# Kernel optimization log

Hardware: AMD Instinct MI355X
Metric: run time of the kernel (lower is better)

## Reference

```python
import jax, jax.numpy as jnp
import numpy as np

B, D = 4096, 512
N_PROTO = 1000          # prototype tasks
CLS_PER_TASK = 10       # indices*10 block size in original code
N_CLASSES = N_PROTO * CLS_PER_TASK
NUM_TEST = 10


def setup_inputs() -> dict:
    key = jax.random.key(0)
    k1, k2, k3 = jax.random.split(key, 3)
    img = jax.random.normal(k1, (B, D), dtype=jnp.float32)
    # image encoder output is L2-normalized and detached in the original
    image_features = img / jnp.linalg.norm(img, axis=-1, keepdims=True)
    ima_proto = jax.random.normal(k2, (N_PROTO, D), dtype=jnp.float32)
    ima_proto = ima_proto / jnp.linalg.norm(ima_proto, axis=-1, keepdims=True)
    text_features_raw = jax.random.normal(k3, (N_CLASSES, D), dtype=jnp.float32)
    logit_scale = jnp.asarray(np.log(1.0 / 0.07), dtype=jnp.float32)  # CLIP init
    return {
        "image_features": image_features,
        "ima_proto": ima_proto,
        "text_features_raw": text_features_raw,
        "logit_scale": logit_scale,
        "num_test": NUM_TEST,
    }


def reference(image_features, ima_proto, text_features_raw, logit_scale, num_test):
    n_proto = ima_proto.shape[0]
    n_classes = text_features_raw.shape[0]
    b = image_features.shape[0]
    k = min(int(num_test), n_proto)

    # probability = image_features @ ima_proto.t(); topk indices
    probability = image_features @ ima_proto.T                      # [B, n_proto]
    _, indices = jax.lax.top_k(probability, k)                      # [B, k]

    # text_features normalized, logit = image_features @ text_features.t()
    text_features = text_features_raw / jnp.linalg.norm(
        text_features_raw, axis=-1, keepdims=True)
    logit = image_features @ text_features.T                        # [B, n_classes]

    # vectorized form of the double loop:
    #   logits[j][idx*10 : idx*10+10] = logit[j][idx*10 : idx*10+10]
    sel = jnp.zeros((b, n_proto), dtype=logit.dtype)
    sel = sel.at[jnp.arange(b)[:, None], indices].set(1.0)          # [B, n_proto]
    block_of_class = jnp.arange(n_classes) // CLS_PER_TASK          # [n_classes]
    mask = sel[:, block_of_class]                                   # [B, n_classes]

    logits = jnp.exp(logit_scale) * (logit * mask)
    return logits
```

## Files before the change

kernel.cpp:

```cpp
#include <hip/hip_runtime.h>
#include <cfloat>
#include <math.h>

#define B_ROWS   4096
#define DIM      512
#define NPROTO   1000
#define NCLASSES 10000
#define KSEL     10
#define KCAND    12
#define CAP      256
#define PROB_LD  1024

#define PROB_BYTES 8388608u
#define OUT_BYTES  163840000u

#define GBM 64
#define GBN 128
#define GBK 32
#define ALD 40

typedef short s16x8 __attribute__((ext_vector_type(8)));
typedef float f32x4 __attribute__((ext_vector_type(4)));

static __device__ __forceinline__ unsigned short f2bf(float f) {
  unsigned int x = __float_as_uint(f);
  return (unsigned short)((x + 0x7fffu + ((x >> 16) & 1u)) >> 16);
}
static __device__ __forceinline__ s16x8 cvt8(float4 a, float4 b) {
  s16x8 r;
  r[0]=f2bf(a.x); r[1]=f2bf(a.y); r[2]=f2bf(a.z); r[3]=f2bf(a.w);
  r[4]=f2bf(b.x); r[5]=f2bf(b.y); r[6]=f2bf(b.z); r[7]=f2bf(b.w);
  return r;
}
static __device__ __forceinline__ unsigned short f2h(float f) {
  _Float16 h = (_Float16)f;
  return __builtin_bit_cast(unsigned short, h);
}
static __device__ __forceinline__ unsigned mono16(unsigned h) {
  return (h & 0x8000u) ? (~h & 0xffffu) : (h | 0x8000u);
}

__global__ __launch_bounds__(256) void k_gemm(
    const float* __restrict__ img, const float* __restrict__ proto,
    unsigned short* __restrict__ prob, int* __restrict__ counts)
{
  __shared__ short Al[GBM * ALD];
  __shared__ short Bl[GBN * ALD];

  const int tid  = threadIdx.x;
  const int lane = tid & 63, wave = tid >> 6;
  const int wr = wave >> 1, wc = wave & 1;
  const int row0 = blockIdx.x * GBM;
  const int col0 = blockIdx.y * GBN;

  const int sr = tid >> 2;
  const int sc = (tid & 3) * 8;

  int pa = col0 + sr;      if (pa > NPROTO - 1) pa = NPROTO - 1;
  int pb = col0 + 64 + sr; if (pb > NPROTO - 1) pb = NPROTO - 1;
  const float* gA  = img   + (size_t)(row0 + sr) * DIM + sc;
  const float* gB0 = proto + (size_t)pa * DIM + sc;
  const float* gB1 = proto + (size_t)pb * DIM + sc;

  float4 ra0  = *(const float4*)(gA);      float4 ra1  = *(const float4*)(gA + 4);
  float4 rb00 = *(const float4*)(gB0);     float4 rb01 = *(const float4*)(gB0 + 4);
  float4 rb10 = *(const float4*)(gB1);     float4 rb11 = *(const float4*)(gB1 + 4);

  f32x4 acc[2][4];
#pragma unroll
  for (int m = 0; m < 2; ++m)
#pragma unroll
    for (int n = 0; n < 4; ++n) acc[m][n] = (f32x4)0.f;

  const int kg = lane >> 4;
  const int fr = lane & 15;

  for (int kt = 0; kt < DIM / GBK; ++kt) {
    *(s16x8*)&Al[sr * ALD + sc]        = cvt8(ra0, ra1);
    *(s16x8*)&Bl[sr * ALD + sc]        = cvt8(rb00, rb01);
    *(s16x8*)&Bl[(64 + sr) * ALD + sc] = cvt8(rb10, rb11);
    __syncthreads();

    if (kt + 1 < DIM / GBK) {
      const int k0 = (kt + 1) * GBK;
      ra0  = *(const float4*)(gA + k0);   ra1  = *(const float4*)(gA + k0 + 4);
      rb00 = *(const float4*)(gB0 + k0);  rb01 = *(const float4*)(gB0 + k0 + 4);
      rb10 = *(const float4*)(gB1 + k0);  rb11 = *(const float4*)(gB1 + k0 + 4);
    }

    s16x8 af[2], bf[4];
#pragma unroll
    for (int m = 0; m < 2; ++m)
      af[m] = *(const s16x8*)&Al[(wr * 32 + m * 16 + fr) * ALD + kg * 8];
#pragma unroll
    for (int n = 0; n < 4; ++n)
      bf[n] = *(const s16x8*)&Bl[(wc * 64 + n * 16 + fr) * ALD + kg * 8];
#pragma unroll
    for (int m = 0; m < 2; ++m)
#pragma unroll
      for (int n = 0; n < 4; ++n)
        acc[m][n] = __builtin_amdgcn_mfma_f32_16x16x32_bf16(
            af[m], bf[n], acc[m][n], 0, 0, 0);
    __syncthreads();
  }

#pragma unroll
  for (int m = 0; m < 2; ++m)
#pragma unroll
    for (int n = 0; n < 4; ++n) {
      const int r = row0 + wr * 32 + m * 16 + (lane >> 4) * 4;
      const int c = col0 + wc * 64 + n * 16 + fr;
#pragma unroll
      for (int reg = 0; reg < 4; ++reg)
        prob[(size_t)(r + reg) * PROB_LD + c] = f2h(acc[m][n][reg]);
    }

  if (blockIdx.x == 0 && blockIdx.y == 0)
    for (int i = tid; i < NPROTO; i += 256) counts[i] = 0;
}

__global__ __launch_bounds__(256) void k_select(
    const unsigned short* __restrict__ prob, const float* __restrict__ img,
    const float* __restrict__ proto, int* __restrict__ counts,
    int* __restrict__ buckets)
{
  const int tid  = threadIdx.x;
  const int wave = tid >> 6, lane = tid & 63;
  const int row  = blockIdx.x * 4 + wave;

  unsigned cand[16];
  {
    const uint4* pu = reinterpret_cast<const uint4*>(
        prob + (size_t)row * PROB_LD) + lane * 2;
    const uint4 w0 = pu[0], w1 = pu[1];
    const unsigned w[8] = {w0.x, w0.y, w0.z, w0.w, w1.x, w1.y, w1.z, w1.w};
    const int cbase = lane * 16;
#pragma unroll
    for (int r = 0; r < 8; ++r) {
      const int c0 = cbase + r * 2;
      const unsigned lo = w[r] & 0xffffu, hi = w[r] >> 16;
      cand[r * 2]     = (c0     < NPROTO) ? ((mono16(lo) << 16) | (0xffffu - c0))       : 0u;
      cand[r * 2 + 1] = (c0 + 1 < NPROTO) ? ((mono16(hi) << 16) | (0xffffu - (c0 + 1))) : 0u;
    }
  }

  int ci[KCAND];
#pragma unroll
  for (int kk = 0; kk < KCAND; ++kk) {
    unsigned best = cand[0];
#pragma unroll
    for (int r = 1; r < 16; ++r) best = max(best, cand[r]);
#pragma unroll
    for (int off = 32; off; off >>= 1)
      best = max(best, (unsigned)__shfl_xor((int)best, off));
    ci[kk] = 0xffff - (int)(best & 0xffffu);
#pragma unroll
    for (int r = 0; r < 16; ++r)
      if (cand[r] == best) cand[r] = 0u;
  }

  const float4* a4 = reinterpret_cast<const float4*>(img + (size_t)row * DIM);
  const float4 a0 = a4[lane], a1 = a4[64 + lane];
  float dv[KCAND];
#pragma unroll
  for (int j = 0; j < KCAND; ++j) {
    const float4* p4 = reinterpret_cast<const float4*>(proto + (size_t)ci[j] * DIM);
    const float4 b0 = p4[lane], b1 = p4[64 + lane];
    float s = 0.f;
    s = fmaf(a0.x, b0.x, s); s = fmaf(a0.y, b0.y, s);
    s = fmaf(a0.z, b0.z, s); s = fmaf(a0.w, b0.w, s);
    s = fmaf(a1.x, b1.x, s); s = fmaf(a1.y, b1.y, s);
    s = fmaf(a1.z, b1.z, s); s = fmaf(a1.w, b1.w, s);
#pragma unroll
    for (int off = 32; off; off >>= 1) s += __shfl_xor(s, off);
    dv[j] = s;
  }

  unsigned picked = 0;
  for (int kk = 0; kk < KSEL; ++kk) {
    float bv = -FLT_MAX;
    int   bj = 0;
#pragma unroll
    for (int j = 0; j < KCAND; ++j)
      if (!((picked >> j) & 1u) && dv[j] > bv) { bv = dv[j]; bj = j; }
    picked |= 1u << bj;
    if (lane == kk) {
      const int pp  = ci[bj];
      const int pos = atomicAdd(&counts[pp], 1);
      if (pos < CAP) buckets[pp * CAP + pos] = row;
    }
  }
}

__global__ __launch_bounds__(256) void k_compute(
    const float* __restrict__ img, const float* __restrict__ text,
    const int* __restrict__ counts, const int* __restrict__ buckets,
    const float* __restrict__ logit_scale, float* __restrict__ out)
{
  __shared__ float stext[KSEL * DIM];
  __shared__ float sfac[KSEL];

  const int p    = blockIdx.x;
  const int tid  = threadIdx.x;
  const int wave = tid >> 6, lane = tid & 63;

  {
    const float4* src = reinterpret_cast<const float4*>(text + (size_t)p * KSEL * DIM);
    float4* dst = reinterpret_cast<float4*>(stext);
#pragma unroll
    for (int i = 0; i < 5; ++i) dst[tid + i * 256] = src[tid + i * 256];
  }
  __syncthreads();

  const float scale = expf(logit_scale[0]);
#pragma unroll
  for (int j = wave; j < KSEL; j += 4) {
    const float4* t4 = reinterpret_cast<const float4*>(stext + j * DIM);
    float4 v0 = t4[lane], v1 = t4[64 + lane];
    float s = 0.f;
    s = fmaf(v0.x, v0.x, s); s = fmaf(v0.y, v0.y, s);
    s = fmaf(v0.z, v0.z, s); s = fmaf(v0.w, v0.w, s);
    s = fmaf(v1.x, v1.x, s); s = fmaf(v1.y, v1.y, s);
    s = fmaf(v1.z, v1.z, s); s = fmaf(v1.w, v1.w, s);
#pragma unroll
    for (int off = 32; off; off >>= 1) s += __shfl_down(s, off);
    if (lane == 0) sfac[j] = scale / sqrtf(s);
  }
  __syncthreads();

  const int n = min(counts[p], CAP);
  const float4* st4 = reinterpret_cast<const float4*>(stext);
  const int* bkt = buckets + p * CAP;

  int row = -1, nrow;
  float4 a0, a1, na0, na1;
  if (wave < n) {
    row = bkt[wave];
    const float4* a4 = reinterpret_cast<const float4*>(img + (size_t)row * DIM);
    a0 = a4[lane]; a1 = a4[64 + lane];
  }

  for (int i = wave; i < n; i += 4) {
    const int inext = i + 4;
    if (inext < n) {
      nrow = bkt[inext];
      const float4* a4 = reinterpret_cast<const float4*>(img + (size_t)nrow * DIM);
      na0 = a4[lane]; na1 = a4[64 + lane];
    }

    float acc[KSEL];
#pragma unroll
    for (int j = 0; j < KSEL; ++j) {
      const float4 b0 = st4[j * 128 + lane];
      const float4 b1 = st4[j * 128 + 64 + lane];
      float s = 0.f;
      s = fmaf(a0.x, b0.x, s); s = fmaf(a0.y, b0.y, s);
      s = fmaf(a0.z, b0.z, s); s = fmaf(a0.w, b0.w, s);
      s = fmaf(a1.x, b1.x, s); s = fmaf(a1.y, b1.y, s);
      s = fmaf(a1.z, b1.z, s); s = fmaf(a1.w, b1.w, s);
      acc[j] = s;
    }
#pragma unroll
    for (int j = 0; j < KSEL; ++j) {
#pragma unroll
      for (int off = 32; off; off >>= 1)
        acc[j] += __shfl_xor(acc[j], off);
    }
    float v = acc[0];
#pragma unroll
    for (int j = 1; j < KSEL; ++j) if (lane == j) v = acc[j];
    if (lane < KSEL)
      out[(size_t)row * NCLASSES + p * KSEL + lane] = v * sfac[lane];

    row = nrow; a0 = na0; a1 = na1;
  }
}

extern "C" void kernel_launch(void* const* d_in, const int* in_sizes, int n_in,
                              void* d_out, int out_size, void* d_ws, size_t ws_size,
                              hipStream_t stream) {
  const float* img    = (const float*)d_in[0];
  const float* proto  = (const float*)d_in[1];
  const float* text   = (const float*)d_in[2];
  const float* lscale = (const float*)d_in[3];

  unsigned short* prob = (unsigned short*)d_out;
  float* out = (float*)d_out;

  int* counts  = (int*)d_ws;
  int* buckets = (int*)((char*)d_ws + 4096);

  k_gemm<<<dim3(B_ROWS / GBM, 1024 / GBN), 256, 0, stream>>>(
      img, proto, prob, counts);
  k_select<<<B_ROWS / 4, 256, 0, stream>>>(prob, img, proto, counts, buckets);
  hipMemsetAsync(d_out, 0, OUT_BYTES, stream);
  k_compute<<<NPROTO, 256, 0, stream>>>(img, text, counts, buckets, lscale, out);
}
```

Baseline: 105.2 us.

## Replace output memset plus scattered writes with a dense per-row output kernel

Drops the full-output memset followed by scattered 10-float writes. k_compute now writes compact per-row top-k results into a workspace buffer, and a new k_out kernel builds each output row in shared memory, zero-filled, then streams it out with non-temporal vector stores. The goal is a single coalesced write pass over the 164MB output instead of a memset plus random partial-line writes. The cost is an extra kernel launch and extra workspace traffic for the top-k indices and values.

```diff
diff --git a/kernel.cpp b/kernel.cpp
--- a/kernel.cpp
+++ b/kernel.cpp
@@ -12,7 +12,6 @@
 #define PROB_LD  1024
 
 #define PROB_BYTES 8388608u
-#define OUT_BYTES  163840000u
 
 #define GBM 64
 #define GBN 128
@@ -122,7 +121,7 @@
 __global__ __launch_bounds__(256) void k_select(
     const unsigned short* __restrict__ prob, const float* __restrict__ img,
     const float* __restrict__ proto, int* __restrict__ counts,
-    int* __restrict__ buckets)
+    int* __restrict__ buckets, int* __restrict__ topk)
 {
   const int tid  = threadIdx.x;
   const int wave = tid >> 6, lane = tid & 63;
@@ -186,8 +185,9 @@
     picked |= 1u << bj;
     if (lane == kk) {
       const int pp  = ci[bj];
+      topk[(size_t)row * KSEL + kk] = pp;
       const int pos = atomicAdd(&counts[pp], 1);
-      if (pos < CAP) buckets[pp * CAP + pos] = row;
+      if (pos < CAP) buckets[pp * CAP + pos] = (row << 4) | kk;
     }
   }
 }
@@ -195,7 +195,7 @@
 __global__ __launch_bounds__(256) void k_compute(
     const float* __restrict__ img, const float* __restrict__ text,
     const int* __restrict__ counts, const int* __restrict__ buckets,
-    const float* __restrict__ logit_scale, float* __restrict__ out)
+    const float* __restrict__ logit_scale, float* __restrict__ vals)
 {
   __shared__ float stext[KSEL * DIM];
   __shared__ float sfac[KSEL];
@@ -232,19 +232,19 @@
   const float4* st4 = reinterpret_cast<const float4*>(stext);
   const int* bkt = buckets + p * CAP;
 
-  int row = -1, nrow;
+  int ent = 0, nent;
   float4 a0, a1, na0, na1;
   if (wave < n) {
-    row = bkt[wave];
-    const float4* a4 = reinterpret_cast<const float4*>(img + (size_t)row * DIM);
+    ent = bkt[wave];
+    const float4* a4 = reinterpret_cast<const float4*>(img + (size_t)(ent >> 4) * DIM);
     a0 = a4[lane]; a1 = a4[64 + lane];
   }
 
   for (int i = wave; i < n; i += 4) {
     const int inext = i + 4;
     if (inext < n) {
-      nrow = bkt[inext];
-      const float4* a4 = reinterpret_cast<const float4*>(img + (size_t)nrow * DIM);
+      nent = bkt[inext];
+      const float4* a4 = reinterpret_cast<const float4*>(img + (size_t)(nent >> 4) * DIM);
       na0 = a4[lane]; na1 = a4[64 + lane];
     }
 
@@ -270,9 +270,43 @@
 #pragma unroll
     for (int j = 1; j < KSEL; ++j) if (lane == j) v = acc[j];
     if (lane < KSEL)
-      out[(size_t)row * NCLASSES + p * KSEL + lane] = v * sfac[lane];
-
-    row = nrow; a0 = na0; a1 = na1;
+      vals[(size_t)(ent >> 4) * (KSEL * KSEL) + (ent & 15) * KSEL + lane]
+          = v * sfac[lane];
+
+    ent = nent; a0 = na0; a1 = na1;
+  }
+}
+
+__global__ __launch_bounds__(256) void k_out(
+    const int* __restrict__ topk, const float* __restrict__ vals,
+    float* __restrict__ out)
+{
+  __shared__ float srow[NCLASSES];
+
+  const int row = blockIdx.x;
+  const int tid = threadIdx.x;
+
+  f32x4* s4 = reinterpret_cast<f32x4*>(srow);
+#pragma unroll
+  for (int i = 0; i < 10; ++i) {
+    const int idx = tid + i * 256;
+    if (idx < NCLASSES / 4) s4[idx] = (f32x4)0.f;
+  }
+  __syncthreads();
+
+  if (tid < KSEL * KSEL) {
+    const int kk = tid / KSEL, j = tid % KSEL;
+    const int col = topk[(size_t)row * KSEL + kk] * KSEL + j;
+    srow[col] = vals[(size_t)row * (KSEL * KSEL) + tid];
+  }
+  __syncthreads();
+
+  f32x4* orow = reinterpret_cast<f32x4*>(out + (size_t)row * NCLASSES);
+#pragma unroll
+  for (int i = 0; i < 10; ++i) {
+    const int idx = tid + i * 256;
+    if (idx < NCLASSES / 4)
+      __builtin_nontemporal_store(s4[idx], orow + idx);
   }
 }
 
@@ -287,12 +321,16 @@
   unsigned short* prob = (unsigned short*)d_out;
   float* out = (float*)d_out;
 
-  int* counts  = (int*)d_ws;
-  int* buckets = (int*)((char*)d_ws + 4096);
+  int*   counts  = (int*)d_ws;
+  int*   buckets = (int*)((char*)d_ws + 4096);
+  int*   topk    = (int*)((char*)d_ws + 4096 + 1024000);
+  float* vals    = (float*)((char*)d_ws + 4096 + 1024000 + 163840);
 
   k_gemm<<<dim3(B_ROWS / GBM, 1024 / GBN), 256, 0, stream>>>(
       img, proto, prob, counts);
-  k_select<<<B_ROWS / 4, 256, 0, stream>>>(prob, img, proto, counts, buckets);
-  hipMemsetAsync(d_out, 0, OUT_BYTES, stream);
-  k_compute<<<NPROTO, 256, 0, stream>>>(img, text, counts, buckets, lscale, out);
-}
+  k_select<<<B_ROWS / 4, 256, 0, stream>>>(
+      prob, img, proto, counts, buckets, topk);
+  k_compute<<<NPROTO, 256, 0, stream>>>(
+      img, text, counts, buckets, lscale, vals);
+  k_out<<<B_ROWS, 256, 0, stream>>>(topk, vals, out);
+}
```

New measurement: 113.6 us. 1.08x slower.
